# Optimization experiments

Measured on AMD Instinct MI355X. Metric: run time of the kernel, lower is better.

The kernel has to match this reference:

```python
import jax, jax.numpy as jnp
import numpy as np

B, S, F, H, A = 2, 2048, 1024, 16, 64


def setup_inputs() -> dict:
    key = jax.random.key(0)
    ks = jax.random.split(key, 6)
    return {
        "key_input": jax.random.normal(ks[0], (B, S, F), dtype=jnp.float32),
        "query_input": jax.random.normal(ks[1], (B, S, F), dtype=jnp.float32),
        "value_input": jax.random.normal(ks[2], (B, S, F), dtype=jnp.float32),
        "q_w": jax.random.normal(ks[3], (H, F, A), dtype=jnp.float32) * (1.0 / np.sqrt(F)),
        "k_w": jax.random.normal(ks[4], (H, F, A), dtype=jnp.float32) * (1.0 / np.sqrt(F)),
        "v_w": jax.random.normal(ks[5], (H, F, A), dtype=jnp.float32) * (1.0 / np.sqrt(F)),
    }


def reference(key_input, query_input, value_input, q_w, k_w, v_w):
    attention_len = q_w.shape[-1]
    # per-head QKV projections: [B,S,F] x [H,F,A] -> [B,S,H,A]
    keys = jnp.einsum('bsf,hfa->bsha', key_input, k_w)
    queries = jnp.einsum('bsf,hfa->bsha', query_input, q_w)
    values = jnp.einsum('bsf,hfa->bsha', value_input, v_w)
    # scores: [B,H,Q,K]; NOTE: original softmaxes over dim=2 (the query axis)
    energy = jnp.einsum('bqha,bkha->bhqk', queries, keys) / jnp.sqrt(
        jnp.asarray(attention_len, dtype=queries.dtype))
    scores = jax.nn.softmax(energy, axis=2)
    # NOTE: original einsum 'bhqs,bsha->bsha' sums over q, keeps s aligned with values
    return jnp.einsum('bhqs,bsha->bsha', scores, values)
```

## Files before the change

### kernel.cpp

```cpp
#include <hip/hip_runtime.h>
#include <hip/hip_bf16.h>

typedef __bf16 bf16_t;
typedef __bf16 bf16x4 __attribute__((ext_vector_type(4)));
typedef __bf16 bf16x8 __attribute__((ext_vector_type(8)));
typedef float  f32x4  __attribute__((ext_vector_type(4)));

typedef __attribute__((address_space(1))) const void  gvoid_t;
typedef __attribute__((address_space(3))) void        lvoid_t;

static constexpr int Mtot = 4096;
static constexpr int Ntot = 1024;
static constexpr int Ktot = 1024;


__global__ __launch_bounds__(256)
void prepass_kernel(const float* __restrict__ A, const float* __restrict__ W,
                    bf16_t* __restrict__ Ab, bf16_t* __restrict__ Wt)
{
    __shared__ float wtile[64][65];
    const int bid = blockIdx.x, t = threadIdx.x;

    if (bid < 1024) {
        const size_t base = (size_t)bid * 4096 + t * 4;
#pragma unroll
        for (int r = 0; r < 4; ++r) {
            const size_t i = base + (size_t)r * 1024;
            const f32x4 v = *(const f32x4*)(A + i);
            bf16x4 p = {(bf16_t)v[0], (bf16_t)v[1], (bf16_t)v[2], (bf16_t)v[3]};
            *(bf16x4*)(Ab + i) = p;
        }
    } else {
        const int wb = bid - 1024;
        const int head = wb >> 4;
        const int k0 = (wb & 15) * 64;
        const float* wsrc = W + (size_t)head * (Ktot * 64) + (size_t)k0 * 64;
#pragma unroll
        for (int i = 0; i < 4; ++i) {
            const int idx = i * 256 + t;
            const int kr = idx >> 4, a4 = (idx & 15) * 4;
            const f32x4 v = *(const f32x4*)(wsrc + (size_t)kr * 64 + a4);
            wtile[kr][a4 + 0] = v[0]; wtile[kr][a4 + 1] = v[1];
            wtile[kr][a4 + 2] = v[2]; wtile[kr][a4 + 3] = v[3];
        }
        __syncthreads();
#pragma unroll
        for (int i = 0; i < 4; ++i) {
            const int idx = i * 256 + t;
            const int ar = idx >> 4, kc = (idx & 15) * 4;
            bf16x4 p = {(bf16_t)wtile[kc + 0][ar], (bf16_t)wtile[kc + 1][ar],
                        (bf16_t)wtile[kc + 2][ar], (bf16_t)wtile[kc + 3][ar]};
            *(bf16x4*)(Wt + (size_t)(head * 64 + ar) * Ktot + k0 + kc) = p;
        }
    }
}

__global__ __launch_bounds__(256, 2)
void gemm_bf16_kernel(const bf16_t* __restrict__ Ab, const bf16_t* __restrict__ Bt,
                      float* __restrict__ C)
{
    __shared__ bf16_t As[2][64 * 64];
    __shared__ bf16_t Bs[2][128 * 64];

    const int t = threadIdx.x, lane = t & 63, wave = t >> 6;
    const int wm = wave & 1, wn = wave >> 1;

    const int g = (blockIdx.x & 7) * 64 + (blockIdx.x >> 3);
    const int by = g >> 3, bx = g & 7;
    const int bm = by * 64, bn = bx * 128;

    const int lrow = lane & 15;
    const int lq   = lane >> 4;

    f32x4 acc[2][4];
#pragma unroll
    for (int mf = 0; mf < 2; ++mf)
#pragma unroll
        for (int nf = 0; nf < 4; ++nf) {
            f32x4 z = {0.f, 0.f, 0.f, 0.f};
            acc[mf][nf] = z;
        }

    auto STAGE = [&](int buf, int k0) {
#pragma unroll
        for (int j = 0; j < 2; ++j) {
            const int chunk = (wave * 2 + j) * 64 + lane;
            const int row = chunk >> 3;
            const int kb  = ((chunk & 7) ^ (row & 7)) * 8;
            const bf16_t* gp = Ab + (size_t)(bm + row) * Ktot + k0 + kb;
            __builtin_amdgcn_global_load_lds((gvoid_t*)gp,
                (lvoid_t*)&As[buf][(wave * 2 + j) * 512], 16, 0, 0);
        }
#pragma unroll
        for (int j = 0; j < 4; ++j) {
            const int chunk = (wave * 4 + j) * 64 + lane;
            const int row = chunk >> 3;
            const int kb  = ((chunk & 7) ^ (row & 7)) * 8;
            const bf16_t* gp = Bt + (size_t)(bn + row) * Ktot + k0 + kb;
            __builtin_amdgcn_global_load_lds((gvoid_t*)gp,
                (lvoid_t*)&Bs[buf][(wave * 4 + j) * 512], 16, 0, 0);
        }
    };

    STAGE(0, 0);
    __syncthreads();

    constexpr int NT = Ktot / 64;
    for (int tI = 0; tI < NT; ++tI) {
        const int cur = tI & 1;
        if (tI + 1 < NT) STAGE(cur ^ 1, (tI + 1) * 64);

#pragma unroll
        for (int kk = 0; kk < 2; ++kk) {
            const int c16 = kk * 4 + lq;
            bf16x8 af[2], bfr[4];
#pragma unroll
            for (int mf = 0; mf < 2; ++mf) {
                const int R = wm * 32 + mf * 16 + lrow;
                af[mf] = *(const bf16x8*)&As[cur][R * 64 + (c16 ^ (R & 7)) * 8];
            }
#pragma unroll
            for (int nf = 0; nf < 4; ++nf) {
                const int R = wn * 64 + nf * 16 + lrow;
                bfr[nf] = *(const bf16x8*)&Bs[cur][R * 64 + (c16 ^ (R & 7)) * 8];
            }
            __builtin_amdgcn_s_setprio(1);
#pragma unroll
            for (int mf = 0; mf < 2; ++mf)
#pragma unroll
                for (int nf = 0; nf < 4; ++nf)
                    acc[mf][nf] = __builtin_amdgcn_mfma_f32_16x16x32_bf16(
                        af[mf], bfr[nf], acc[mf][nf], 0, 0, 0);
            __builtin_amdgcn_s_setprio(0);
        }
        __syncthreads();
    }

#pragma unroll
    for (int mf = 0; mf < 2; ++mf) {
        const int row0 = bm + wm * 32 + mf * 16 + (lq << 2);
#pragma unroll
        for (int nf = 0; nf < 4; ++nf) {
            const int col = bn + wn * 64 + nf * 16 + lrow;
#pragma unroll
            for (int i = 0; i < 4; ++i)
                C[(size_t)(row0 + i) * Ntot + col] = acc[mf][nf][i];
        }
    }
}

static constexpr int FBM = 128, FBN = 128, FBK = 64, FBKP = 72;

__global__ __launch_bounds__(512, 2)
void vproj_fused_kernel(const float* __restrict__ A, const float* __restrict__ W,
                        float* __restrict__ C)
{
    __shared__ bf16_t As[2][FBM][FBKP];
    __shared__ bf16_t Bs[2][FBN][FBKP];

    const int t = threadIdx.x, lane = t & 63, wave = t >> 6;
    const int wm = wave >> 2, wn = wave & 3;
    const int tile = (blockIdx.x & 7) * 32 + (blockIdx.x >> 3);
    const int bm = (tile >> 3) * FBM, bn = (tile & 7) * FBN;

    const int bhead = t >> 8, brem = t & 255;
    const int bkq = brem >> 4, baq = brem & 15;
    const float* const wbase = W + ((size_t)((bn >> 6) + bhead)) * (Ktot * 64)
                                 + (size_t)(bkq * 4) * 64 + baq * 4;
    f32x4 avreg[4], bvreg[4];

    auto load_tile = [&](int k0) {
#pragma unroll
        for (int r = 0; r < 4; ++r) {
            const int idx = r * 512 + t;
            avreg[r] = *(const f32x4*)(A + (size_t)(bm + (idx >> 4)) * Ktot + k0 + (idx & 15) * 4);
        }
        const float* wp = wbase + (size_t)k0 * 64;
#pragma unroll
        for (int r = 0; r < 4; ++r) bvreg[r] = *(const f32x4*)(wp + r * 64);
    };
    auto store_tile = [&](int buf) {
#pragma unroll
        for (int r = 0; r < 4; ++r) {
            const int idx = r * 512 + t;
            bf16x4 p = {(bf16_t)avreg[r][0], (bf16_t)avreg[r][1],
                        (bf16_t)avreg[r][2], (bf16_t)avreg[r][3]};
            *(bf16x4*)&As[buf][idx >> 4][(idx & 15) * 4] = p;
        }
#pragma unroll
        for (int j = 0; j < 4; ++j) {
            bf16x4 p = {(bf16_t)bvreg[0][j], (bf16_t)bvreg[1][j],
                        (bf16_t)bvreg[2][j], (bf16_t)bvreg[3][j]};
            *(bf16x4*)&Bs[buf][bhead * 64 + baq * 4 + j][bkq * 4] = p;
        }
    };

    f32x4 acc[4][2];
#pragma unroll
    for (int mf = 0; mf < 4; ++mf)
#pragma unroll
        for (int nf = 0; nf < 2; ++nf) { f32x4 z = {0,0,0,0}; acc[mf][nf] = z; }

    const int lrow = lane & 15, lkb = (lane >> 4) << 3;
    load_tile(0); store_tile(0); __syncthreads();

    for (int tI = 0; tI < Ktot / FBK; ++tI) {
        const int cur = tI & 1;
        if (tI + 1 < Ktot / FBK) load_tile((tI + 1) * FBK);
#pragma unroll
        for (int kk = 0; kk < 2; ++kk) {
            bf16x8 af[4], bfr[2];
#pragma unroll
            for (int mf = 0; mf < 4; ++mf)
                af[mf] = *(const bf16x8*)&As[cur][wm * 64 + mf * 16 + lrow][kk * 32 + lkb];
#pragma unroll
            for (int nf = 0; nf < 2; ++nf)
                bfr[nf] = *(const bf16x8*)&Bs[cur][wn * 32 + nf * 16 + lrow][kk * 32 + lkb];
#pragma unroll
            for (int mf = 0; mf < 4; ++mf)
#pragma unroll
                for (int nf = 0; nf < 2; ++nf)
                    acc[mf][nf] = __builtin_amdgcn_mfma_f32_16x16x32_bf16(
                        af[mf], bfr[nf], acc[mf][nf], 0, 0, 0);
        }
        if (tI + 1 < Ktot / FBK) store_tile(cur ^ 1);
        __syncthreads();
    }
#pragma unroll
    for (int mf = 0; mf < 4; ++mf) {
        const int row0 = bm + wm * 64 + mf * 16 + ((lane >> 4) << 2);
#pragma unroll
        for (int nf = 0; nf < 2; ++nf) {
            const int col = bn + wn * 32 + nf * 16 + (lane & 15);
#pragma unroll
            for (int i = 0; i < 4; ++i)
                C[(size_t)(row0 + i) * Ntot + col] = acc[mf][nf][i];
        }
    }
}

extern "C" void kernel_launch(void* const* d_in, const int* in_sizes, int n_in,
                              void* d_out, int out_size, void* d_ws, size_t ws_size,
                              hipStream_t stream) {
    (void)in_sizes; (void)n_in; (void)out_size;
    const float* V  = (const float*)d_in[2];
    const float* Vw = (const float*)d_in[5];
    float* out      = (float*)d_out;

    const size_t abBytes = (size_t)Mtot * Ktot * sizeof(bf16_t);
    const size_t wtBytes = (size_t)Ntot * Ktot * sizeof(bf16_t);

    if (ws_size >= abBytes + wtBytes) {
        bf16_t* Ab = (bf16_t*)d_ws;
        bf16_t* Wt = (bf16_t*)((char*)d_ws + abBytes);
        hipLaunchKernelGGL(prepass_kernel, dim3(1024 + 256), dim3(256), 0, stream,
                           V, Vw, Ab, Wt);
        hipLaunchKernelGGL(gemm_bf16_kernel, dim3((Mtot / 64) * (Ntot / 128)),
                           dim3(256), 0, stream, Ab, Wt, out);
    } else {
        hipLaunchKernelGGL(vproj_fused_kernel, dim3(256), dim3(512), 0, stream,
                           V, Vw, out);
    }
}
```

Measured before the change: 28.31 us.

## Drop activation bf16 prepass; load fp32 A directly into LDS and convert in GEMM

Removes the prepass that converted the value input to bf16. The GEMM now streams fp32 activations into LDS with a swizzled layout and converts them to bf16 when building MFMA fragments. It also restructures the double-buffered loop to use explicit waitcnt and s_barrier around the prefetch. This saves a full read and write of the bf16 activation copy plus a kernel's worth of work. In exchange the GEMM reads twice as many A bytes per tile, uses more LDS, and adds conversion ALU work in the inner loop.

```diff
diff --git a/kernel.cpp b/kernel.cpp
--- a/kernel.cpp
+++ b/kernel.cpp
@@ -15,51 +15,37 @@
 
 
 __global__ __launch_bounds__(256)
-void prepass_kernel(const float* __restrict__ A, const float* __restrict__ W,
-                    bf16_t* __restrict__ Ab, bf16_t* __restrict__ Wt)
+void prepass_w_kernel(const float* __restrict__ W, bf16_t* __restrict__ Wt)
 {
     __shared__ float wtile[64][65];
-    const int bid = blockIdx.x, t = threadIdx.x;
-
-    if (bid < 1024) {
-        const size_t base = (size_t)bid * 4096 + t * 4;
-#pragma unroll
-        for (int r = 0; r < 4; ++r) {
-            const size_t i = base + (size_t)r * 1024;
-            const f32x4 v = *(const f32x4*)(A + i);
-            bf16x4 p = {(bf16_t)v[0], (bf16_t)v[1], (bf16_t)v[2], (bf16_t)v[3]};
-            *(bf16x4*)(Ab + i) = p;
-        }
-    } else {
-        const int wb = bid - 1024;
-        const int head = wb >> 4;
-        const int k0 = (wb & 15) * 64;
-        const float* wsrc = W + (size_t)head * (Ktot * 64) + (size_t)k0 * 64;
-#pragma unroll
-        for (int i = 0; i < 4; ++i) {
-            const int idx = i * 256 + t;
-            const int kr = idx >> 4, a4 = (idx & 15) * 4;
-            const f32x4 v = *(const f32x4*)(wsrc + (size_t)kr * 64 + a4);
-            wtile[kr][a4 + 0] = v[0]; wtile[kr][a4 + 1] = v[1];
-            wtile[kr][a4 + 2] = v[2]; wtile[kr][a4 + 3] = v[3];
-        }
-        __syncthreads();
-#pragma unroll
-        for (int i = 0; i < 4; ++i) {
-            const int idx = i * 256 + t;
-            const int ar = idx >> 4, kc = (idx & 15) * 4;
-            bf16x4 p = {(bf16_t)wtile[kc + 0][ar], (bf16_t)wtile[kc + 1][ar],
-                        (bf16_t)wtile[kc + 2][ar], (bf16_t)wtile[kc + 3][ar]};
-            *(bf16x4*)(Wt + (size_t)(head * 64 + ar) * Ktot + k0 + kc) = p;
-        }
+    const int wb = blockIdx.x, t = threadIdx.x;
+    const int head = wb >> 4;
+    const int k0 = (wb & 15) * 64;
+    const float* wsrc = W + (size_t)head * (Ktot * 64) + (size_t)k0 * 64;
+#pragma unroll
+    for (int i = 0; i < 4; ++i) {
+        const int idx = i * 256 + t;
+        const int kr = idx >> 4, a4 = (idx & 15) * 4;
+        const f32x4 v = *(const f32x4*)(wsrc + (size_t)kr * 64 + a4);
+        wtile[kr][a4 + 0] = v[0]; wtile[kr][a4 + 1] = v[1];
+        wtile[kr][a4 + 2] = v[2]; wtile[kr][a4 + 3] = v[3];
+    }
+    __syncthreads();
+#pragma unroll
+    for (int i = 0; i < 4; ++i) {
+        const int idx = i * 256 + t;
+        const int ar = idx >> 4, kc = (idx & 15) * 4;
+        bf16x4 p = {(bf16_t)wtile[kc + 0][ar], (bf16_t)wtile[kc + 1][ar],
+                    (bf16_t)wtile[kc + 2][ar], (bf16_t)wtile[kc + 3][ar]};
+        *(bf16x4*)(Wt + (size_t)(head * 64 + ar) * Ktot + k0 + kc) = p;
     }
 }
 
 __global__ __launch_bounds__(256, 2)
-void gemm_bf16_kernel(const bf16_t* __restrict__ Ab, const bf16_t* __restrict__ Bt,
-                      float* __restrict__ C)
+void gemm_mixed_kernel(const float* __restrict__ A, const bf16_t* __restrict__ Bt,
+                       float* __restrict__ C)
 {
-    __shared__ bf16_t As[2][64 * 64];
+    __shared__ float  As[2][64 * 64];
     __shared__ bf16_t Bs[2][128 * 64];
 
     const int t = threadIdx.x, lane = t & 63, wave = t >> 6;
@@ -83,46 +69,45 @@
 
     auto STAGE = [&](int buf, int k0) {
 #pragma unroll
-        for (int j = 0; j < 2; ++j) {
-            const int chunk = (wave * 2 + j) * 64 + lane;
-            const int row = chunk >> 3;
-            const int kb  = ((chunk & 7) ^ (row & 7)) * 8;
-            const bf16_t* gp = Ab + (size_t)(bm + row) * Ktot + k0 + kb;
+        for (int j = 0; j < 4; ++j) {
+            const int chunk = (wave * 4 + j) * 64 + lane;
+            const int row = chunk >> 4;
+            const int kc  = ((chunk & 15) ^ (row & 7)) << 2;
+            const float* gp = A + (size_t)(bm + row) * Ktot + k0 + kc;
             __builtin_amdgcn_global_load_lds((gvoid_t*)gp,
-                (lvoid_t*)&As[buf][(wave * 2 + j) * 512], 16, 0, 0);
+                (lvoid_t*)&As[buf][(wave * 4 + j) * 256], 16, 0, 0);
         }
 #pragma unroll
         for (int j = 0; j < 4; ++j) {
             const int chunk = (wave * 4 + j) * 64 + lane;
             const int row = chunk >> 3;
-            const int kb  = ((chunk & 7) ^ (row & 7)) * 8;
+            const int kb  = ((chunk & 7) ^ (row & 7)) << 3;
             const bf16_t* gp = Bt + (size_t)(bn + row) * Ktot + k0 + kb;
             __builtin_amdgcn_global_load_lds((gvoid_t*)gp,
                 (lvoid_t*)&Bs[buf][(wave * 4 + j) * 512], 16, 0, 0);
         }
     };
 
-    STAGE(0, 0);
-    __syncthreads();
-
-    constexpr int NT = Ktot / 64;
-    for (int tI = 0; tI < NT; ++tI) {
-        const int cur = tI & 1;
-        if (tI + 1 < NT) STAGE(cur ^ 1, (tI + 1) * 64);
-
+    auto COMPUTE = [&](int cur) {
 #pragma unroll
         for (int kk = 0; kk < 2; ++kk) {
             const int c16 = kk * 4 + lq;
+            const int gA  = kk * 8 + lq * 2;
             bf16x8 af[2], bfr[4];
 #pragma unroll
             for (int mf = 0; mf < 2; ++mf) {
                 const int R = wm * 32 + mf * 16 + lrow;
-                af[mf] = *(const bf16x8*)&As[cur][R * 64 + (c16 ^ (R & 7)) * 8];
+                const int x = R & 7;
+                const f32x4 lo = *(const f32x4*)&As[cur][R * 64 + ((gA ^ x) << 2)];
+                const f32x4 hi = *(const f32x4*)&As[cur][R * 64 + (((gA + 1) ^ x) << 2)];
+                bf16x8 v = {(bf16_t)lo[0], (bf16_t)lo[1], (bf16_t)lo[2], (bf16_t)lo[3],
+                            (bf16_t)hi[0], (bf16_t)hi[1], (bf16_t)hi[2], (bf16_t)hi[3]};
+                af[mf] = v;
             }
 #pragma unroll
             for (int nf = 0; nf < 4; ++nf) {
                 const int R = wn * 64 + nf * 16 + lrow;
-                bfr[nf] = *(const bf16x8*)&Bs[cur][R * 64 + (c16 ^ (R & 7)) * 8];
+                bfr[nf] = *(const bf16x8*)&Bs[cur][R * 64 + ((c16 ^ (R & 7)) << 3)];
             }
             __builtin_amdgcn_s_setprio(1);
 #pragma unroll
@@ -133,8 +118,26 @@
                         af[mf], bfr[nf], acc[mf][nf], 0, 0, 0);
             __builtin_amdgcn_s_setprio(0);
         }
-        __syncthreads();
-    }
+    };
+
+    constexpr int NT = Ktot / 64;
+    STAGE(0, 0);
+
+    for (int tI = 0; tI < NT - 1; ++tI) {
+        const int cur = tI & 1;
+        __builtin_amdgcn_s_barrier();
+        STAGE(cur ^ 1, (tI + 1) * 64);
+        asm volatile("s_waitcnt vmcnt(8)" ::: "memory");
+        __builtin_amdgcn_sched_barrier(0);
+        __builtin_amdgcn_s_barrier();
+        __builtin_amdgcn_sched_barrier(0);
+        COMPUTE(cur);
+    }
+    asm volatile("s_waitcnt vmcnt(0)" ::: "memory");
+    __builtin_amdgcn_sched_barrier(0);
+    __builtin_amdgcn_s_barrier();
+    __builtin_amdgcn_sched_barrier(0);
+    COMPUTE((NT - 1) & 1);
 
 #pragma unroll
     for (int mf = 0; mf < 2; ++mf) {
@@ -247,16 +250,13 @@
     const float* Vw = (const float*)d_in[5];
     float* out      = (float*)d_out;
 
-    const size_t abBytes = (size_t)Mtot * Ktot * sizeof(bf16_t);
     const size_t wtBytes = (size_t)Ntot * Ktot * sizeof(bf16_t);
 
-    if (ws_size >= abBytes + wtBytes) {
-        bf16_t* Ab = (bf16_t*)d_ws;
-        bf16_t* Wt = (bf16_t*)((char*)d_ws + abBytes);
-        hipLaunchKernelGGL(prepass_kernel, dim3(1024 + 256), dim3(256), 0, stream,
-                           V, Vw, Ab, Wt);
-        hipLaunchKernelGGL(gemm_bf16_kernel, dim3((Mtot / 64) * (Ntot / 128)),
-                           dim3(256), 0, stream, Ab, Wt, out);
+    if (ws_size >= wtBytes) {
+        bf16_t* Wt = (bf16_t*)d_ws;
+        hipLaunchKernelGGL(prepass_w_kernel, dim3(256), dim3(256), 0, stream, Vw, Wt);
+        hipLaunchKernelGGL(gemm_mixed_kernel, dim3((Mtot / 64) * (Ntot / 128)),
+                           dim3(256), 0, stream, V, Wt, out);
     } else {
         hipLaunchKernelGGL(vproj_fused_kernel, dim3(256), dim3(512), 0, stream,
                            V, Vw, out);
```

New measurement: 28.82 us. Within noise of the previous version (+1.8%).

## Fuse fp32-to-bf16 conversion of activations into the GEMM A-tile load

Applied to the files above, without the earlier changes.

The GEMM now reads the fp32 activations straight from global memory into registers, converts them to bf16 and writes them to shared memory after the compute step. The prepass only converts and transposes the weights. This drops the separate activation conversion pass and its bf16 round trip through memory (write 8MB, reread). In exchange the A tile is loaded through registers instead of direct-to-LDS loads and twice the bytes are fetched per tile. Each A tile is also re-read by all 8 N-blocks, which raises L2 traffic and register pressure. The fallback kernel's stores were also changed from vector to scalar, but that path is unused.

```diff
diff --git a/kernel.cpp b/kernel.cpp
--- a/kernel.cpp
+++ b/kernel.cpp
@@ -15,49 +15,35 @@
 
 
 __global__ __launch_bounds__(256)
-void prepass_kernel(const float* __restrict__ A, const float* __restrict__ W,
-                    bf16_t* __restrict__ Ab, bf16_t* __restrict__ Wt)
+void prepass_w_kernel(const float* __restrict__ W, bf16_t* __restrict__ Wt)
 {
     __shared__ float wtile[64][65];
-    const int bid = blockIdx.x, t = threadIdx.x;
-
-    if (bid < 1024) {
-        const size_t base = (size_t)bid * 4096 + t * 4;
-#pragma unroll
-        for (int r = 0; r < 4; ++r) {
-            const size_t i = base + (size_t)r * 1024;
-            const f32x4 v = *(const f32x4*)(A + i);
-            bf16x4 p = {(bf16_t)v[0], (bf16_t)v[1], (bf16_t)v[2], (bf16_t)v[3]};
-            *(bf16x4*)(Ab + i) = p;
-        }
-    } else {
-        const int wb = bid - 1024;
-        const int head = wb >> 4;
-        const int k0 = (wb & 15) * 64;
-        const float* wsrc = W + (size_t)head * (Ktot * 64) + (size_t)k0 * 64;
-#pragma unroll
-        for (int i = 0; i < 4; ++i) {
-            const int idx = i * 256 + t;
-            const int kr = idx >> 4, a4 = (idx & 15) * 4;
-            const f32x4 v = *(const f32x4*)(wsrc + (size_t)kr * 64 + a4);
-            wtile[kr][a4 + 0] = v[0]; wtile[kr][a4 + 1] = v[1];
-            wtile[kr][a4 + 2] = v[2]; wtile[kr][a4 + 3] = v[3];
-        }
-        __syncthreads();
-#pragma unroll
-        for (int i = 0; i < 4; ++i) {
-            const int idx = i * 256 + t;
-            const int ar = idx >> 4, kc = (idx & 15) * 4;
-            bf16x4 p = {(bf16_t)wtile[kc + 0][ar], (bf16_t)wtile[kc + 1][ar],
-                        (bf16_t)wtile[kc + 2][ar], (bf16_t)wtile[kc + 3][ar]};
-            *(bf16x4*)(Wt + (size_t)(head * 64 + ar) * Ktot + k0 + kc) = p;
-        }
+    const int wb = blockIdx.x, t = threadIdx.x;
+    const int head = wb >> 4;
+    const int k0 = (wb & 15) * 64;
+    const float* wsrc = W + (size_t)head * (Ktot * 64) + (size_t)k0 * 64;
+#pragma unroll
+    for (int i = 0; i < 4; ++i) {
+        const int idx = i * 256 + t;
+        const int kr = idx >> 4, a4 = (idx & 15) * 4;
+        const f32x4 v = *(const f32x4*)(wsrc + (size_t)kr * 64 + a4);
+        wtile[kr][a4 + 0] = v[0]; wtile[kr][a4 + 1] = v[1];
+        wtile[kr][a4 + 2] = v[2]; wtile[kr][a4 + 3] = v[3];
+    }
+    __syncthreads();
+#pragma unroll
+    for (int i = 0; i < 4; ++i) {
+        const int idx = i * 256 + t;
+        const int ar = idx >> 4, kc = (idx & 15) * 4;
+        bf16x4 p = {(bf16_t)wtile[kc + 0][ar], (bf16_t)wtile[kc + 1][ar],
+                    (bf16_t)wtile[kc + 2][ar], (bf16_t)wtile[kc + 3][ar]};
+        *(bf16x4*)(Wt + (size_t)(head * 64 + ar) * Ktot + k0 + kc) = p;
     }
 }
 
 __global__ __launch_bounds__(256, 2)
-void gemm_bf16_kernel(const bf16_t* __restrict__ Ab, const bf16_t* __restrict__ Bt,
-                      float* __restrict__ C)
+void gemm_fusedA_kernel(const float* __restrict__ A, const bf16_t* __restrict__ Bt,
+                        float* __restrict__ C)
 {
     __shared__ bf16_t As[2][64 * 64];
     __shared__ bf16_t Bs[2][128 * 64];
@@ -81,16 +67,35 @@
             acc[mf][nf] = z;
         }
 
-    auto STAGE = [&](int buf, int k0) {
+    int aRow[2], aKb[2];
+#pragma unroll
+    for (int j = 0; j < 2; ++j) {
+        const int chunk = (wave * 2 + j) * 64 + lane;
+        aRow[j] = chunk >> 3;
+        aKb[j]  = ((chunk & 7) ^ (aRow[j] & 7)) * 8;
+    }
+    f32x4 aReg[2][2];
+
+    auto LOADA = [&](int k0) {
 #pragma unroll
         for (int j = 0; j < 2; ++j) {
-            const int chunk = (wave * 2 + j) * 64 + lane;
-            const int row = chunk >> 3;
-            const int kb  = ((chunk & 7) ^ (row & 7)) * 8;
-            const bf16_t* gp = Ab + (size_t)(bm + row) * Ktot + k0 + kb;
-            __builtin_amdgcn_global_load_lds((gvoid_t*)gp,
-                (lvoid_t*)&As[buf][(wave * 2 + j) * 512], 16, 0, 0);
-        }
+            const float* ap = A + (size_t)(bm + aRow[j]) * Ktot + k0 + aKb[j];
+            aReg[j][0] = *(const f32x4*)(ap);
+            aReg[j][1] = *(const f32x4*)(ap + 4);
+        }
+    };
+    auto WRITEA = [&](int buf) {
+#pragma unroll
+        for (int j = 0; j < 2; ++j) {
+            bf16x8 v = {(bf16_t)aReg[j][0][0], (bf16_t)aReg[j][0][1],
+                        (bf16_t)aReg[j][0][2], (bf16_t)aReg[j][0][3],
+                        (bf16_t)aReg[j][1][0], (bf16_t)aReg[j][1][1],
+                        (bf16_t)aReg[j][1][2], (bf16_t)aReg[j][1][3]};
+            *(bf16x8*)&As[buf][(wave * 2 + j) * 512 + lane * 8] = v;
+        }
+    };
+
+    auto STAGEB = [&](int buf, int k0) {
 #pragma unroll
         for (int j = 0; j < 4; ++j) {
             const int chunk = (wave * 4 + j) * 64 + lane;
@@ -102,14 +107,7 @@
         }
     };
 
-    STAGE(0, 0);
-    __syncthreads();
-
-    constexpr int NT = Ktot / 64;
-    for (int tI = 0; tI < NT; ++tI) {
-        const int cur = tI & 1;
-        if (tI + 1 < NT) STAGE(cur ^ 1, (tI + 1) * 64);
-
+    auto COMPUTE = [&](int cur) {
 #pragma unroll
         for (int kk = 0; kk < 2; ++kk) {
             const int c16 = kk * 4 + lq;
@@ -117,12 +115,12 @@
 #pragma unroll
             for (int mf = 0; mf < 2; ++mf) {
                 const int R = wm * 32 + mf * 16 + lrow;
-                af[mf] = *(const bf16x8*)&As[cur][R * 64 + (c16 ^ (R & 7)) * 8];
+                af[mf] = *(const bf16x8*)&As[cur][R * 64 + ((c16 ^ (R & 7)) << 3)];
             }
 #pragma unroll
             for (int nf = 0; nf < 4; ++nf) {
                 const int R = wn * 64 + nf * 16 + lrow;
-                bfr[nf] = *(const bf16x8*)&Bs[cur][R * 64 + (c16 ^ (R & 7)) * 8];
+                bfr[nf] = *(const bf16x8*)&Bs[cur][R * 64 + ((c16 ^ (R & 7)) << 3)];
             }
             __builtin_amdgcn_s_setprio(1);
 #pragma unroll
@@ -133,6 +131,22 @@
                         af[mf], bfr[nf], acc[mf][nf], 0, 0, 0);
             __builtin_amdgcn_s_setprio(0);
         }
+    };
+
+    LOADA(0);
+    WRITEA(0);
+    STAGEB(0, 0);
+    __syncthreads();
+
+    constexpr int NT = Ktot / 64;
+    for (int tI = 0; tI < NT; ++tI) {
+        const int cur = tI & 1;
+        if (tI + 1 < NT) {
+            LOADA((tI + 1) * 64);
+            STAGEB(cur ^ 1, (tI + 1) * 64);
+        }
+        COMPUTE(cur);
+        if (tI + 1 < NT) WRITEA(cur ^ 1);
         __syncthreads();
     }
 
@@ -183,15 +197,15 @@
 #pragma unroll
         for (int r = 0; r < 4; ++r) {
             const int idx = r * 512 + t;
-            bf16x4 p = {(bf16_t)avreg[r][0], (bf16_t)avreg[r][1],
-                        (bf16_t)avreg[r][2], (bf16_t)avreg[r][3]};
-            *(bf16x4*)&As[buf][idx >> 4][(idx & 15) * 4] = p;
+            bf16_t* dst = &As[buf][idx >> 4][(idx & 15) * 4];
+            dst[0] = (bf16_t)avreg[r][0]; dst[1] = (bf16_t)avreg[r][1];
+            dst[2] = (bf16_t)avreg[r][2]; dst[3] = (bf16_t)avreg[r][3];
         }
 #pragma unroll
         for (int j = 0; j < 4; ++j) {
-            bf16x4 p = {(bf16_t)bvreg[0][j], (bf16_t)bvreg[1][j],
-                        (bf16_t)bvreg[2][j], (bf16_t)bvreg[3][j]};
-            *(bf16x4*)&Bs[buf][bhead * 64 + baq * 4 + j][bkq * 4] = p;
+            bf16_t* dst = &Bs[buf][bhead * 64 + baq * 4 + j][bkq * 4];
+            dst[0] = (bf16_t)bvreg[0][j]; dst[1] = (bf16_t)bvreg[1][j];
+            dst[2] = (bf16_t)bvreg[2][j]; dst[3] = (bf16_t)bvreg[3][j];
         }
     };
 
@@ -247,16 +261,13 @@
     const float* Vw = (const float*)d_in[5];
     float* out      = (float*)d_out;
 
-    const size_t abBytes = (size_t)Mtot * Ktot * sizeof(bf16_t);
     const size_t wtBytes = (size_t)Ntot * Ktot * sizeof(bf16_t);
 
-    if (ws_size >= abBytes + wtBytes) {
-        bf16_t* Ab = (bf16_t*)d_ws;
-        bf16_t* Wt = (bf16_t*)((char*)d_ws + abBytes);
-        hipLaunchKernelGGL(prepass_kernel, dim3(1024 + 256), dim3(256), 0, stream,
-                           V, Vw, Ab, Wt);
-        hipLaunchKernelGGL(gemm_bf16_kernel, dim3((Mtot / 64) * (Ntot / 128)),
-                           dim3(256), 0, stream, Ab, Wt, out);
+    if (ws_size >= wtBytes) {
+        bf16_t* Wt = (bf16_t*)d_ws;
+        hipLaunchKernelGGL(prepass_w_kernel, dim3(256), dim3(256), 0, stream, Vw, Wt);
+        hipLaunchKernelGGL(gemm_fusedA_kernel, dim3((Mtot / 64) * (Ntot / 128)),
+                           dim3(256), 0, stream, V, Wt, out);
     } else {
         hipLaunchKernelGGL(vproj_fused_kernel, dim3(256), dim3(512), 0, stream,
                            V, Vw, out);
```

After: 29.48 us. 4.1% more time.

## Restructure GEMM K-loop with explicit vmcnt waits and split barriers

Applied to the files above, without the earlier changes.

The bf16 GEMM main loop is reorganized into a prologue, a steady state and an epilogue. Each iteration issues the next tile's global-to-LDS loads, waits with s_waitcnt vmcnt(6) only for the current tile's loads, and then barriers, so the prefetch stays in flight during compute. The intent is to remove the full drain at the per-iteration __syncthreads. Separately, the fused V-projection kernel now writes its LDS stores as scalar bf16 elements instead of bf16x4 vector stores. That may generate more LDS store instructions and cost performance.

```diff
diff --git a/kernel.cpp b/kernel.cpp
--- a/kernel.cpp
+++ b/kernel.cpp
@@ -102,14 +102,7 @@
         }
     };
 
-    STAGE(0, 0);
-    __syncthreads();
-
-    constexpr int NT = Ktot / 64;
-    for (int tI = 0; tI < NT; ++tI) {
-        const int cur = tI & 1;
-        if (tI + 1 < NT) STAGE(cur ^ 1, (tI + 1) * 64);
-
+    auto COMPUTE = [&](int cur) {
 #pragma unroll
         for (int kk = 0; kk < 2; ++kk) {
             const int c16 = kk * 4 + lq;
@@ -117,12 +110,12 @@
 #pragma unroll
             for (int mf = 0; mf < 2; ++mf) {
                 const int R = wm * 32 + mf * 16 + lrow;
-                af[mf] = *(const bf16x8*)&As[cur][R * 64 + (c16 ^ (R & 7)) * 8];
+                af[mf] = *(const bf16x8*)&As[cur][R * 64 + ((c16 ^ (R & 7)) << 3)];
             }
 #pragma unroll
             for (int nf = 0; nf < 4; ++nf) {
                 const int R = wn * 64 + nf * 16 + lrow;
-                bfr[nf] = *(const bf16x8*)&Bs[cur][R * 64 + (c16 ^ (R & 7)) * 8];
+                bfr[nf] = *(const bf16x8*)&Bs[cur][R * 64 + ((c16 ^ (R & 7)) << 3)];
             }
             __builtin_amdgcn_s_setprio(1);
 #pragma unroll
@@ -133,8 +126,26 @@
                         af[mf], bfr[nf], acc[mf][nf], 0, 0, 0);
             __builtin_amdgcn_s_setprio(0);
         }
-        __syncthreads();
-    }
+    };
+
+    constexpr int NT = Ktot / 64;
+    STAGE(0, 0);
+
+    for (int tI = 0; tI < NT - 1; ++tI) {
+        const int cur = tI & 1;
+        __builtin_amdgcn_s_barrier();
+        STAGE(cur ^ 1, (tI + 1) * 64);
+        asm volatile("s_waitcnt vmcnt(6)" ::: "memory");
+        __builtin_amdgcn_sched_barrier(0);
+        __builtin_amdgcn_s_barrier();
+        __builtin_amdgcn_sched_barrier(0);
+        COMPUTE(cur);
+    }
+    asm volatile("s_waitcnt vmcnt(0)" ::: "memory");
+    __builtin_amdgcn_sched_barrier(0);
+    __builtin_amdgcn_s_barrier();
+    __builtin_amdgcn_sched_barrier(0);
+    COMPUTE((NT - 1) & 1);
 
 #pragma unroll
     for (int mf = 0; mf < 2; ++mf) {
@@ -183,15 +194,15 @@
 #pragma unroll
         for (int r = 0; r < 4; ++r) {
             const int idx = r * 512 + t;
-            bf16x4 p = {(bf16_t)avreg[r][0], (bf16_t)avreg[r][1],
-                        (bf16_t)avreg[r][2], (bf16_t)avreg[r][3]};
-            *(bf16x4*)&As[buf][idx >> 4][(idx & 15) * 4] = p;
+            bf16_t* dst = &As[buf][idx >> 4][(idx & 15) * 4];
+            dst[0] = (bf16_t)avreg[r][0]; dst[1] = (bf16_t)avreg[r][1];
+            dst[2] = (bf16_t)avreg[r][2]; dst[3] = (bf16_t)avreg[r][3];
         }
 #pragma unroll
         for (int j = 0; j < 4; ++j) {
-            bf16x4 p = {(bf16_t)bvreg[0][j], (bf16_t)bvreg[1][j],
-                        (bf16_t)bvreg[2][j], (bf16_t)bvreg[3][j]};
-            *(bf16x4*)&Bs[buf][bhead * 64 + baq * 4 + j][bkq * 4] = p;
+            bf16_t* dst = &Bs[buf][bhead * 64 + baq * 4 + j][bkq * 4];
+            dst[0] = (bf16_t)bvreg[0][j]; dst[1] = (bf16_t)bvreg[1][j];
+            dst[2] = (bf16_t)bvreg[2][j]; dst[3] = (bf16_t)bvreg[3][j];
         }
     };
 
```

Measured after the change: 30.14 us, median of 5. 6.5% more time.
